# Optimization experiments

Measured on AMD Instinct MI355X. Metric: run time of the kernel, lower is better.

Reference implementation:

```python
import jax, jax.numpy as jnp
import numpy as np

NUM_HEADS = 8

B, N, M = 2, 10000, 320000
QD = KD = HD = 256


def setup_inputs() -> dict:
    key = jax.random.key(0)
    k1, k2, k3, k4, k5 = jax.random.split(key, 5)
    x_q = jax.random.normal(k1, (B, N, QD), dtype=jnp.float32)
    x_k = jax.random.normal(k2, (B, N, KD), dtype=jnp.float32)
    mask = jax.random.randint(k3, (2, M), 0, N, dtype=jnp.int64)
    # xavier_uniform: limit = sqrt(6/(fan_in+fan_out))
    lim_q = float(np.sqrt(6.0 / (QD + HD)))
    lim_k = float(np.sqrt(6.0 / (KD + HD)))
    w_q = jax.random.uniform(k4, (QD, HD), minval=-lim_q, maxval=lim_q, dtype=jnp.float32)
    w_k = jax.random.uniform(k5, (KD, HD), minval=-lim_k, maxval=lim_k, dtype=jnp.float32)
    return {"x_q": x_q, "x_k": x_k, "mask": mask, "w_q": w_q, "w_k": w_k}


def reference(x_q, x_k, mask, w_q, w_k):
    b, n, _ = x_q.shape
    m = mask.shape[1]
    d = w_q.shape[1]          # hidden_dim
    h = NUM_HEADS
    dh = d // h
    q = x_q @ w_q             # (b, n, d)
    k = x_k @ w_k             # (b, n, d)
    # edge gather + elementwise multiply
    prod = q[:, mask[0], :] * k[:, mask[1], :]            # (b, m, d)
    # head buffer is i // (d/h): contiguous blocks -> reshape-sum
    a = prod.reshape(b, m, h, dh).sum(axis=-1)            # (b, m, h)
    a = a / jnp.sqrt(jnp.float32(w_k.shape[0]))           # / sqrt(key_dim)
    # segment softmax over destination index = mask[1 - reduce_dim], reduce_dim=1 -> mask[0]
    idx = mask[0]
    a = a - a.max()                                       # global max, as in source
    e = jnp.exp(a)                                        # (b, m, h)
    seg = jnp.zeros((b, n, h), e.dtype).at[:, idx, :].add(e)
    return e / (seg[:, idx, :] + 1e-16)
```

## Files before the change

kernel.cpp:

```cpp
#include <hip/hip_runtime.h>
#include <hip/hip_bf16.h>
#include <hip/hip_fp16.h>

#define DHID 256
#define NHEAD 8
#define BATCH 2
#define PAD 96

typedef _Float16 h8 __attribute__((ext_vector_type(8)));
typedef _Float16 h2 __attribute__((ext_vector_type(2)));
typedef float f4 __attribute__((ext_vector_type(4)));
typedef int i2 __attribute__((ext_vector_type(2)));

__global__ __launch_bounds__(256) void prep_kernel(
    const float* __restrict__ Wq, const float* __restrict__ Wk,
    _Float16* __restrict__ Wfq, _Float16* __restrict__ Wfk,
    int* __restrict__ cnt, int N)
{
    if (blockIdx.z == 2) {
        const int gid = (blockIdx.y * 8 + blockIdx.x) * 256
                      + threadIdx.y * 32 + threadIdx.x;
        if (gid < N) cnt[gid] = 0;
        return;
    }
    const float* W = blockIdx.z ? Wk : Wq;
    _Float16* Wf   = blockIdx.z ? Wfk : Wfq;
    __shared__ float tile[32][33];
    const int tx = threadIdx.x;
    const int ty = threadIdx.y;
    const int n0 = blockIdx.x * 32;
    const int k0 = blockIdx.y * 32;
#pragma unroll
    for (int j = 0; j < 32; j += 8)
        tile[ty + j][tx] = W[(size_t)(k0 + ty + j) * DHID + n0 + tx];
    __syncthreads();
#pragma unroll
    for (int j = 0; j < 32; j += 8) {
        const int n = n0 + ty + j;
        const int k = k0 + tx;
        const size_t u = ((size_t)(n >> 4) * 32 + (k >> 3)) * 16 + (n & 15);
        Wf[u * 8 + (k & 7)] = (_Float16)tile[tx][ty + j];
    }
}

__global__ __launch_bounds__(256, 4) void gemm_mfma(
    const float* __restrict__ Xq, const float* __restrict__ Xk,
    const _Float16* __restrict__ Wfq, const _Float16* __restrict__ Wfk,
    _Float16* __restrict__ Qh, _Float16* __restrict__ Kh,
    const int* __restrict__ mask, int* __restrict__ cnt, int* __restrict__ sde,
    int nx, int Mrows, int M, int N)
{
    const int t = threadIdx.x;
    if ((int)blockIdx.x >= nx) {
        const int sb = ((int)blockIdx.x - nx) + (blockIdx.z ? 64 : 0);
        for (int e = sb * 256 + t; e < M; e += 128 * 256) {
            int s = mask[e];
            int r = atomicAdd(&cnt[s], 1);
            if (r < PAD) {
                i2 v; v[0] = mask[M + e]; v[1] = e;
                *(i2*)(sde + ((size_t)s * PAD + r) * 2) = v;
            }
        }
        return;
    }

    const float* X     = blockIdx.z ? Xk : Xq;
    const _Float16* Wf = blockIdx.z ? Wfk : Wfq;
    _Float16* C        = blockIdx.z ? Kh : Qh;

    const int lane = t & 63;
    const int wave = t >> 6;
    const int quad = lane >> 4;
    const int l16  = lane & 15;
    const int rowBase = blockIdx.x * 64;
    int arow = rowBase + wave * 16 + l16;
    if (arow >= Mrows) arow = Mrows - 1;

    h8 af[8];
#pragma unroll
    for (int kc = 0; kc < 8; ++kc) {
        const float* p = X + (size_t)arow * DHID + (kc * 4 + quad) * 8;
        f4 v0 = *(const f4*)p;
        f4 v1 = *(const f4*)(p + 4);
        h8 hv;
        hv[0]=(_Float16)v0[0]; hv[1]=(_Float16)v0[1]; hv[2]=(_Float16)v0[2]; hv[3]=(_Float16)v0[3];
        hv[4]=(_Float16)v1[0]; hv[5]=(_Float16)v1[1]; hv[6]=(_Float16)v1[2]; hv[7]=(_Float16)v1[3];
        af[kc] = hv;
    }

#pragma unroll 1
    for (int ct64 = 0; ct64 < 4; ++ct64) {
        f4 acc[4] = {{0,0,0,0},{0,0,0,0},{0,0,0,0},{0,0,0,0}};
#pragma unroll
        for (int kc = 0; kc < 8; ++kc) {
#pragma unroll
            for (int ct = 0; ct < 4; ++ct) {
                const h8 bf = *(const h8*)(Wf +
                    (((size_t)(ct64 * 4 + ct) * 32 + kc * 4 + quad) * 16 + l16) * 8);
                acc[ct] = __builtin_amdgcn_mfma_f32_16x16x32_f16(af[kc], bf, acc[ct], 0, 0, 0);
            }
        }
#pragma unroll
        for (int ct = 0; ct < 4; ++ct) {
#pragma unroll
            for (int r = 0; r < 4; ++r) {
                int grow = rowBase + wave * 16 + quad * 4 + r;
                if (grow < Mrows) {
                    int bb = grow >= N;
                    int nn = grow - (bb ? N : 0);
                    C[((size_t)nn * 2 + bb) * DHID + ct64 * 64 + ct * 16 + l16]
                        = (_Float16)acc[ct][r];
                }
            }
        }
    }
}

__global__ __launch_bounds__(256, 8) void edge_kernel(
    const _Float16* __restrict__ Qh, const _Float16* __restrict__ Kh,
    const int* __restrict__ cnt, const int* __restrict__ sde,
    float* __restrict__ out, int M, int N)
{
    __shared__ _Float16 evs[4][PAD][2][NHEAD];
    const int lane = threadIdx.x & 63;
    const int wave = threadIdx.x >> 6;
    const int c    = lane & 31;
    const int half = lane >> 5;
    const int h    = c >> 2;
    const int src  = blockIdx.x * 4 + wave;
    if (src >= N) return;
    int deg = cnt[src];
    if (deg > PAD) deg = PAD;
    if (deg == 0) return;
    const size_t base = (size_t)src * PAD;

    int dstv = 0, eidv = 0;
    if (lane < deg) {
        i2 v = *(const i2*)(sde + (base + lane) * 2);
        dstv = v[0]; eidv = v[1];
    }

    const _Float16* Qrow = Qh + (size_t)src * 2 * DHID;
    const h8 q0 = *(const h8*)(Qrow + c * 8);
    const h8 q1 = *(const h8*)(Qrow + DHID + c * 8);

    float seg0 = 0.f, seg1 = 0.f;
    for (int it = 0; it < deg; it += 8) {
        int pl[4], dd[4];
#pragma unroll
        for (int p = 0; p < 4; ++p) {
            pl[p] = it + p * 2 + half;
            if (it < 64) {
                dd[p] = __shfl(dstv, pl[p]);
            } else {
                int sc = pl[p] < deg ? pl[p] : deg - 1;
                dd[p] = sde[(base + sc) * 2];
            }
        }
        h8 k0v[4], k1v[4];
#pragma unroll
        for (int p = 0; p < 4; ++p) {
            const _Float16* Krow = Kh + (size_t)dd[p] * 2 * DHID;
            k0v[p] = *(const h8*)(Krow + c * 8);
            k1v[p] = *(const h8*)(Krow + DHID + c * 8);
        }
#pragma unroll
        for (int p = 0; p < 4; ++p) {
            float s0 = 0.f, s1 = 0.f;
#if __has_builtin(__builtin_amdgcn_fdot2)
#pragma unroll
            for (int u = 0; u < 4; ++u) {
                h2 a0, b0, a1, b1;
                a0[0] = q0[2*u];      a0[1] = q0[2*u+1];
                b0[0] = k0v[p][2*u];  b0[1] = k0v[p][2*u+1];
                a1[0] = q1[2*u];      a1[1] = q1[2*u+1];
                b1[0] = k1v[p][2*u];  b1[1] = k1v[p][2*u+1];
                s0 = __builtin_amdgcn_fdot2(a0, b0, s0, false);
                s1 = __builtin_amdgcn_fdot2(a1, b1, s1, false);
            }
#else
#pragma unroll
            for (int u = 0; u < 8; ++u) {
                s0 += (float)q0[u] * (float)k0v[p][u];
                s1 += (float)q1[u] * (float)k1v[p][u];
            }
#endif
            s0 += __shfl_xor(s0, 1); s0 += __shfl_xor(s0, 2);
            s1 += __shfl_xor(s1, 1); s1 += __shfl_xor(s1, 2);
            if ((c & 3) == 0 && pl[p] < deg) {
                _Float16 e0 = (_Float16)expf(s0 * 0.0625f);
                _Float16 e1 = (_Float16)expf(s1 * 0.0625f);
                evs[wave][pl[p]][0][h] = e0;
                evs[wave][pl[p]][1][h] = e1;
                seg0 += (float)e0; seg1 += (float)e1;
            }
        }
    }

    seg0 += __shfl_xor(seg0, 32);
    seg1 += __shfl_xor(seg1, 32);
    const float r0 = __builtin_amdgcn_rcpf(seg0 + 1e-16f);
    const float r1 = __builtin_amdgcn_rcpf(seg1 + 1e-16f);

    for (int it = 0; it < deg; it += 8) {
        int pl[4], ee[4];
#pragma unroll
        for (int p = 0; p < 4; ++p) {
            pl[p] = it + p * 2 + half;
            if (it < 64) {
                ee[p] = __shfl(eidv, pl[p]);
            } else {
                int sc = pl[p] < deg ? pl[p] : deg - 1;
                ee[p] = sde[(base + sc) * 2 + 1];
            }
        }
#pragma unroll
        for (int p = 0; p < 4; ++p) {
            if ((c & 3) == 0 && pl[p] < deg) {
                float v0 = (float)evs[wave][pl[p]][0][h] * r0;
                float v1 = (float)evs[wave][pl[p]][1][h] * r1;
                __builtin_nontemporal_store(v0, &out[(size_t)ee[p] * NHEAD + h]);
                __builtin_nontemporal_store(v1,
                    &out[(size_t)M * NHEAD + (size_t)ee[p] * NHEAD + h]);
            }
        }
    }
}

extern "C" void kernel_launch(void* const* d_in, const int* in_sizes, int n_in,
                              void* d_out, int out_size, void* d_ws, size_t ws_size,
                              hipStream_t stream) {
    const float* x_q  = (const float*)d_in[0];
    const float* x_k  = (const float*)d_in[1];
    const int*   mask = (const int*)d_in[2];
    const float* w_q  = (const float*)d_in[3];
    const float* w_k  = (const float*)d_in[4];
    float* out = (float*)d_out;

    const int M = in_sizes[2] / 2;
    const int N = in_sizes[0] / (BATCH * DHID);
    const int Mrows = BATCH * N;

    _Float16* Qh  = (_Float16*)d_ws;
    _Float16* Kh  = Qh  + (size_t)Mrows * DHID;
    _Float16* Wfq = Kh  + (size_t)Mrows * DHID;
    _Float16* Wfk = Wfq + (size_t)DHID * DHID;
    int*      cnt = (int*)(Wfk + (size_t)DHID * DHID);
    int*      sde = cnt + N;

    prep_kernel<<<dim3(DHID / 32, DHID / 32, 3), dim3(32, 8), 0, stream>>>(
        w_q, w_k, Wfq, Wfk, cnt, N);

    const int nx = (Mrows + 63) / 64;
    gemm_mfma<<<dim3(nx + 64, 1, 2), 256, 0, stream>>>(
        x_q, x_k, Wfq, Wfk, Qh, Kh, mask, cnt, sde, nx, Mrows, M, N);

    edge_kernel<<<dim3((N + 3) / 4), 256, 0, stream>>>(
        Qh, Kh, cnt, sde, out, M, N);
}
```

Measured before the change: 171.6 us.

## Prefetch next K-row gathers in edge kernel and split GEMM tiles across waves

The edge kernel now double-buffers its K-row gathers, loading the next group of 8 edges' K vectors before computing dot products on the current group. This hides gather latency at the cost of more registers, so the occupancy hint drops from 8 to 4 blocks. The exp call switches to the fast __expf intrinsic. The GEMM now gives each block 32 rows, with waves splitting the column tiles in pairs, which doubles the block count to spread the projection across more CUs.

After: 177.0 us. 1.03x slower.

```diff
diff --git a/kernel.cpp b/kernel.cpp
--- a/kernel.cpp
+++ b/kernel.cpp
@@ -72,8 +72,10 @@
     const int wave = t >> 6;
     const int quad = lane >> 4;
     const int l16  = lane & 15;
-    const int rowBase = blockIdx.x * 64;
-    int arow = rowBase + wave * 16 + l16;
+    const int rowHalf = wave & 1;
+    const int ctPair  = wave >> 1;
+    const int rowBase = blockIdx.x * 32;
+    int arow = rowBase + rowHalf * 16 + l16;
     if (arow >= Mrows) arow = Mrows - 1;
 
     h8 af[8];
@@ -88,8 +90,9 @@
         af[kc] = hv;
     }
 
-#pragma unroll 1
-    for (int ct64 = 0; ct64 < 4; ++ct64) {
+#pragma unroll
+    for (int cc = 0; cc < 2; ++cc) {
+        const int ct64 = ctPair * 2 + cc;
         f4 acc[4] = {{0,0,0,0},{0,0,0,0},{0,0,0,0},{0,0,0,0}};
 #pragma unroll
         for (int kc = 0; kc < 8; ++kc) {
@@ -104,7 +107,7 @@
         for (int ct = 0; ct < 4; ++ct) {
 #pragma unroll
             for (int r = 0; r < 4; ++r) {
-                int grow = rowBase + wave * 16 + quad * 4 + r;
+                int grow = rowBase + rowHalf * 16 + quad * 4 + r;
                 if (grow < Mrows) {
                     int bb = grow >= N;
                     int nn = grow - (bb ? N : 0);
@@ -116,7 +119,7 @@
     }
 }
 
-__global__ __launch_bounds__(256, 8) void edge_kernel(
+__global__ __launch_bounds__(256, 4) void edge_kernel(
     const _Float16* __restrict__ Qh, const _Float16* __restrict__ Kh,
     const int* __restrict__ cnt, const int* __restrict__ sde,
     float* __restrict__ out, int M, int N)
@@ -144,56 +147,74 @@
     const h8 q0 = *(const h8*)(Qrow + c * 8);
     const h8 q1 = *(const h8*)(Qrow + DHID + c * 8);
 
+    auto get_dd = [&](int it, int* dd) {
+#pragma unroll
+        for (int p = 0; p < 4; ++p) {
+            int pl = it + p * 2 + half;
+            if (it < 64) {
+                dd[p] = __shfl(dstv, pl);
+            } else {
+                int sc = pl < deg ? pl : deg - 1;
+                dd[p] = sde[(base + sc) * 2];
+            }
+        }
+    };
+    auto load_kv = [&](const int* dd, h8* ka, h8* kb) {
+#pragma unroll
+        for (int p = 0; p < 4; ++p) {
+            const _Float16* Krow = Kh + (size_t)dd[p] * 2 * DHID;
+            ka[p] = *(const h8*)(Krow + c * 8);
+            kb[p] = *(const h8*)(Krow + DHID + c * 8);
+        }
+    };
+
     float seg0 = 0.f, seg1 = 0.f;
+    int dd0[4]; h8 ka[4], kb[4];
+    get_dd(0, dd0);
+    load_kv(dd0, ka, kb);
+
     for (int it = 0; it < deg; it += 8) {
-        int pl[4], dd[4];
-#pragma unroll
-        for (int p = 0; p < 4; ++p) {
-            pl[p] = it + p * 2 + half;
-            if (it < 64) {
-                dd[p] = __shfl(dstv, pl[p]);
-            } else {
-                int sc = pl[p] < deg ? pl[p] : deg - 1;
-                dd[p] = sde[(base + sc) * 2];
-            }
-        }
-        h8 k0v[4], k1v[4];
-#pragma unroll
-        for (int p = 0; p < 4; ++p) {
-            const _Float16* Krow = Kh + (size_t)dd[p] * 2 * DHID;
-            k0v[p] = *(const h8*)(Krow + c * 8);
-            k1v[p] = *(const h8*)(Krow + DHID + c * 8);
-        }
-#pragma unroll
-        for (int p = 0; p < 4; ++p) {
+        const int itn = it + 8;
+        int dd1[4]; h8 kna[4], knb[4];
+        const bool more = itn < deg;
+        if (more) { get_dd(itn, dd1); load_kv(dd1, kna, knb); }
+
+#pragma unroll
+        for (int p = 0; p < 4; ++p) {
+            const int pl = it + p * 2 + half;
             float s0 = 0.f, s1 = 0.f;
 #if __has_builtin(__builtin_amdgcn_fdot2)
 #pragma unroll
             for (int u = 0; u < 4; ++u) {
                 h2 a0, b0, a1, b1;
-                a0[0] = q0[2*u];      a0[1] = q0[2*u+1];
-                b0[0] = k0v[p][2*u];  b0[1] = k0v[p][2*u+1];
-                a1[0] = q1[2*u];      a1[1] = q1[2*u+1];
-                b1[0] = k1v[p][2*u];  b1[1] = k1v[p][2*u+1];
+                a0[0] = q0[2*u];     a0[1] = q0[2*u+1];
+                b0[0] = ka[p][2*u];  b0[1] = ka[p][2*u+1];
+                a1[0] = q1[2*u];     a1[1] = q1[2*u+1];
+                b1[0] = kb[p][2*u];  b1[1] = kb[p][2*u+1];
                 s0 = __builtin_amdgcn_fdot2(a0, b0, s0, false);
                 s1 = __builtin_amdgcn_fdot2(a1, b1, s1, false);
             }
 #else
 #pragma unroll
             for (int u = 0; u < 8; ++u) {
-                s0 += (float)q0[u] * (float)k0v[p][u];
-                s1 += (float)q1[u] * (float)k1v[p][u];
+                s0 += (float)q0[u] * (float)ka[p][u];
+                s1 += (float)q1[u] * (float)kb[p][u];
             }
 #endif
             s0 += __shfl_xor(s0, 1); s0 += __shfl_xor(s0, 2);
             s1 += __shfl_xor(s1, 1); s1 += __shfl_xor(s1, 2);
-            if ((c & 3) == 0 && pl[p] < deg) {
-                _Float16 e0 = (_Float16)expf(s0 * 0.0625f);
-                _Float16 e1 = (_Float16)expf(s1 * 0.0625f);
-                evs[wave][pl[p]][0][h] = e0;
-                evs[wave][pl[p]][1][h] = e1;
+            if ((c & 3) == 0 && pl < deg) {
+                _Float16 e0 = (_Float16)__expf(s0 * 0.0625f);
+                _Float16 e1 = (_Float16)__expf(s1 * 0.0625f);
+                evs[wave][pl][0][h] = e0;
+                evs[wave][pl][1][h] = e1;
                 seg0 += (float)e0; seg1 += (float)e1;
             }
+        }
+
+        if (more) {
+#pragma unroll
+            for (int p = 0; p < 4; ++p) { ka[p] = kna[p]; kb[p] = knb[p]; }
         }
     }
 
@@ -251,7 +272,7 @@
     prep_kernel<<<dim3(DHID / 32, DHID / 32, 3), dim3(32, 8), 0, stream>>>(
         w_q, w_k, Wfq, Wfk, cnt, N);
 
-    const int nx = (Mrows + 63) / 64;
+    const int nx = (Mrows + 31) / 32;
     gemm_mfma<<<dim3(nx + 64, 1, 2), 256, 0, stream>>>(
         x_q, x_k, Wfq, Wfk, Qh, Kh, mask, cnt, sde, nx, Mrows, M, N);
 
```

## Split GEMM block into 32-row tiles with per-wave column pairs and double-buffered B loads

Applied to the files above, without the earlier changes.

Each GEMM block now covers 32 rows instead of 64, and its four waves split into two row halves times two column-pair groups, so every wave computes two 64-column tiles rather than four. B-fragment loads are double-buffered with explicit prefetch two k-steps ahead, to overlap global loads with MFMA work. The grid doubles and each X row is loaded by two waves, which raises redundant X traffic in exchange for more parallelism and less latency. The edge kernel also switches expf to the fast __expf intrinsic.

Result: slower. 176.6 us (+3.0%).

```diff
diff --git a/kernel.cpp b/kernel.cpp
--- a/kernel.cpp
+++ b/kernel.cpp
@@ -42,6 +42,22 @@
         Wf[u * 8 + (k & 7)] = (_Float16)tile[tx][ty + j];
     }
 }
+
+#define LOADB(c64, kc, dst)                                                     \
+    do {                                                                        \
+        dst[0] = *(const h8*)(Wf + ((((size_t)(c64) * 4 + 0) * 32 + (kc) * 4 + quad) * 16 + l16) * 8); \
+        dst[1] = *(const h8*)(Wf + ((((size_t)(c64) * 4 + 1) * 32 + (kc) * 4 + quad) * 16 + l16) * 8); \
+        dst[2] = *(const h8*)(Wf + ((((size_t)(c64) * 4 + 2) * 32 + (kc) * 4 + quad) * 16 + l16) * 8); \
+        dst[3] = *(const h8*)(Wf + ((((size_t)(c64) * 4 + 3) * 32 + (kc) * 4 + quad) * 16 + l16) * 8); \
+    } while (0)
+
+#define MFMA4(acc, kc, buf)                                                     \
+    do {                                                                        \
+        acc[0] = __builtin_amdgcn_mfma_f32_16x16x32_f16(af[kc], buf[0], acc[0], 0, 0, 0); \
+        acc[1] = __builtin_amdgcn_mfma_f32_16x16x32_f16(af[kc], buf[1], acc[1], 0, 0, 0); \
+        acc[2] = __builtin_amdgcn_mfma_f32_16x16x32_f16(af[kc], buf[2], acc[2], 0, 0, 0); \
+        acc[3] = __builtin_amdgcn_mfma_f32_16x16x32_f16(af[kc], buf[3], acc[3], 0, 0, 0); \
+    } while (0)
 
 __global__ __launch_bounds__(256, 4) void gemm_mfma(
     const float* __restrict__ Xq, const float* __restrict__ Xk,
@@ -72,8 +88,10 @@
     const int wave = t >> 6;
     const int quad = lane >> 4;
     const int l16  = lane & 15;
-    const int rowBase = blockIdx.x * 64;
-    int arow = rowBase + wave * 16 + l16;
+    const int rowHalf = wave & 1;
+    const int ctPair  = wave >> 1;
+    const int rowBase = blockIdx.x * 32;
+    int arow = rowBase + rowHalf * 16 + l16;
     if (arow >= Mrows) arow = Mrows - 1;
 
     h8 af[8];
@@ -88,29 +106,49 @@
         af[kc] = hv;
     }
 
-#pragma unroll 1
-    for (int ct64 = 0; ct64 < 4; ++ct64) {
-        f4 acc[4] = {{0,0,0,0},{0,0,0,0},{0,0,0,0},{0,0,0,0}};
-#pragma unroll
-        for (int kc = 0; kc < 8; ++kc) {
-#pragma unroll
-            for (int ct = 0; ct < 4; ++ct) {
-                const h8 bf = *(const h8*)(Wf +
-                    (((size_t)(ct64 * 4 + ct) * 32 + kc * 4 + quad) * 16 + l16) * 8);
-                acc[ct] = __builtin_amdgcn_mfma_f32_16x16x32_f16(af[kc], bf, acc[ct], 0, 0, 0);
-            }
-        }
-#pragma unroll
-        for (int ct = 0; ct < 4; ++ct) {
-#pragma unroll
-            for (int r = 0; r < 4; ++r) {
-                int grow = rowBase + wave * 16 + quad * 4 + r;
-                if (grow < Mrows) {
-                    int bb = grow >= N;
-                    int nn = grow - (bb ? N : 0);
-                    C[((size_t)nn * 2 + bb) * DHID + ct64 * 64 + ct * 16 + l16]
-                        = (_Float16)acc[ct][r];
-                }
+    const int c0 = ctPair * 2;
+    const int c1 = c0 + 1;
+    h8 bufA[4], bufB[4];
+    f4 acc0[4] = {{0,0,0,0},{0,0,0,0},{0,0,0,0},{0,0,0,0}};
+    f4 acc1[4] = {{0,0,0,0},{0,0,0,0},{0,0,0,0},{0,0,0,0}};
+
+    LOADB(c0, 0, bufA);
+    LOADB(c0, 1, bufB);
+
+#pragma unroll
+    for (int kc = 0; kc < 8; ++kc) {
+        if ((kc & 1) == 0) {
+            MFMA4(acc0, kc, bufA);
+            if (kc + 2 < 8) { LOADB(c0, kc + 2, bufA); }
+            else            { LOADB(c1, kc - 6, bufA); }
+        } else {
+            MFMA4(acc0, kc, bufB);
+            if (kc + 2 < 8) { LOADB(c0, kc + 2, bufB); }
+            else            { LOADB(c1, kc - 6, bufB); }
+        }
+    }
+#pragma unroll
+    for (int kc = 0; kc < 8; ++kc) {
+        if ((kc & 1) == 0) {
+            MFMA4(acc1, kc, bufA);
+            if (kc + 2 < 8) { LOADB(c1, kc + 2, bufA); }
+        } else {
+            MFMA4(acc1, kc, bufB);
+            if (kc + 2 < 8) { LOADB(c1, kc + 2, bufB); }
+        }
+    }
+
+#pragma unroll
+    for (int ct = 0; ct < 4; ++ct) {
+#pragma unroll
+        for (int r = 0; r < 4; ++r) {
+            int grow = rowBase + rowHalf * 16 + quad * 4 + r;
+            if (grow < Mrows) {
+                int bb = grow >= N;
+                int nn = grow - (bb ? N : 0);
+                size_t rowoff = ((size_t)nn * 2 + bb) * DHID;
+                C[rowoff + c0 * 64 + ct * 16 + l16] = (_Float16)acc0[ct][r];
+                C[rowoff + c1 * 64 + ct * 16 + l16] = (_Float16)acc1[ct][r];
             }
         }
     }
@@ -188,8 +226,8 @@
             s0 += __shfl_xor(s0, 1); s0 += __shfl_xor(s0, 2);
             s1 += __shfl_xor(s1, 1); s1 += __shfl_xor(s1, 2);
             if ((c & 3) == 0 && pl[p] < deg) {
-                _Float16 e0 = (_Float16)expf(s0 * 0.0625f);
-                _Float16 e1 = (_Float16)expf(s1 * 0.0625f);
+                _Float16 e0 = (_Float16)__expf(s0 * 0.0625f);
+                _Float16 e1 = (_Float16)__expf(s1 * 0.0625f);
                 evs[wave][pl[p]][0][h] = e0;
                 evs[wave][pl[p]][1][h] = e1;
                 seg0 += (float)e0; seg1 += (float)e1;
@@ -251,7 +289,7 @@
     prep_kernel<<<dim3(DHID / 32, DHID / 32, 3), dim3(32, 8), 0, stream>>>(
         w_q, w_k, Wfq, Wfk, cnt, N);
 
-    const int nx = (Mrows + 63) / 64;
+    const int nx = (Mrows + 31) / 32;
     gemm_mfma<<<dim3(nx + 64, 1, 2), 256, 0, stream>>>(
         x_q, x_k, Wfq, Wfk, Qh, Kh, mask, cnt, sde, nx, Mrows, M, N);
 
```

## Stage GEMM operands in swizzled LDS tiles instead of register/global fragments

Applied to the files above, without the earlier changes.

The projection GEMM now converts the 64x256 X tile to fp16 into XOR-swizzled shared memory. Per 64-column chunk it loads the plain transposed weight into shared memory as well, and MFMA fragments are read from LDS instead of directly from global memory in a pre-fragmented layout. The intent is cheaper, conflict-free operand fetches. In exchange it adds 64 KB of LDS per block, extra syncthreads, and lowers the launch-bounds occupancy hint to 2. The edge kernel also switches expf to the faster __expf intrinsic.

Result: no change. 169.9 us (-0.9%).

```diff
diff --git a/kernel.cpp b/kernel.cpp
--- a/kernel.cpp
+++ b/kernel.cpp
@@ -14,7 +14,7 @@
 
 __global__ __launch_bounds__(256) void prep_kernel(
     const float* __restrict__ Wq, const float* __restrict__ Wk,
-    _Float16* __restrict__ Wfq, _Float16* __restrict__ Wfk,
+    _Float16* __restrict__ Wtq, _Float16* __restrict__ Wtk,
     int* __restrict__ cnt, int N)
 {
     if (blockIdx.z == 2) {
@@ -24,7 +24,7 @@
         return;
     }
     const float* W = blockIdx.z ? Wk : Wq;
-    _Float16* Wf   = blockIdx.z ? Wfk : Wfq;
+    _Float16* Wt   = blockIdx.z ? Wtk : Wtq;
     __shared__ float tile[32][33];
     const int tx = threadIdx.x;
     const int ty = threadIdx.y;
@@ -35,17 +35,13 @@
         tile[ty + j][tx] = W[(size_t)(k0 + ty + j) * DHID + n0 + tx];
     __syncthreads();
 #pragma unroll
-    for (int j = 0; j < 32; j += 8) {
-        const int n = n0 + ty + j;
-        const int k = k0 + tx;
-        const size_t u = ((size_t)(n >> 4) * 32 + (k >> 3)) * 16 + (n & 15);
-        Wf[u * 8 + (k & 7)] = (_Float16)tile[tx][ty + j];
-    }
-}
-
-__global__ __launch_bounds__(256, 4) void gemm_mfma(
+    for (int j = 0; j < 32; j += 8)
+        Wt[(size_t)(n0 + ty + j) * DHID + k0 + tx] = (_Float16)tile[tx][ty + j];
+}
+
+__global__ __launch_bounds__(256, 2) void gemm_mfma(
     const float* __restrict__ Xq, const float* __restrict__ Xk,
-    const _Float16* __restrict__ Wfq, const _Float16* __restrict__ Wfk,
+    const _Float16* __restrict__ Wtq, const _Float16* __restrict__ Wtk,
     _Float16* __restrict__ Qh, _Float16* __restrict__ Kh,
     const int* __restrict__ mask, int* __restrict__ cnt, int* __restrict__ sde,
     int nx, int Mrows, int M, int N)
@@ -64,42 +60,65 @@
         return;
     }
 
-    const float* X     = blockIdx.z ? Xk : Xq;
-    const _Float16* Wf = blockIdx.z ? Wfk : Wfq;
-    _Float16* C        = blockIdx.z ? Kh : Qh;
+    const float* X       = blockIdx.z ? Xk : Xq;
+    const _Float16* Wt   = blockIdx.z ? Wtk : Wtq;
+    _Float16* C          = blockIdx.z ? Kh : Qh;
+
+    __shared__ _Float16 As[64 * 256];
+    __shared__ _Float16 Bs[64 * 256];
 
     const int lane = t & 63;
     const int wave = t >> 6;
-    const int quad = lane >> 4;
-    const int l16  = lane & 15;
     const int rowBase = blockIdx.x * 64;
-    int arow = rowBase + wave * 16 + l16;
-    if (arow >= Mrows) arow = Mrows - 1;
-
-    h8 af[8];
-#pragma unroll
-    for (int kc = 0; kc < 8; ++kc) {
-        const float* p = X + (size_t)arow * DHID + (kc * 4 + quad) * 8;
-        f4 v0 = *(const f4*)p;
-        f4 v1 = *(const f4*)(p + 4);
+
+#pragma unroll
+    for (int i = 0; i < 8; ++i) {
+        int idx = t + i * 256;
+        int row = idx >> 5;
+        int c   = idx & 31;
+        int grow = rowBase + row;
+        f4 v0 = {0,0,0,0}, v1 = {0,0,0,0};
+        if (grow < Mrows) {
+            const float* p = X + (size_t)grow * DHID + c * 8;
+            v0 = *(const f4*)p;
+            v1 = *(const f4*)(p + 4);
+        }
         h8 hv;
         hv[0]=(_Float16)v0[0]; hv[1]=(_Float16)v0[1]; hv[2]=(_Float16)v0[2]; hv[3]=(_Float16)v0[3];
         hv[4]=(_Float16)v1[0]; hv[5]=(_Float16)v1[1]; hv[6]=(_Float16)v1[2]; hv[7]=(_Float16)v1[3];
-        af[kc] = hv;
-    }
-
-#pragma unroll 1
+        int sc = c ^ (row & 7);
+        *(h8*)&As[row * 256 + sc * 8] = hv;
+    }
+
+    const int ar   = wave * 16 + (lane & 15);
+    const int quad = lane >> 4;
+
     for (int ct64 = 0; ct64 < 4; ++ct64) {
+#pragma unroll
+        for (int i = 0; i < 8; ++i) {
+            int idx = t + i * 256;
+            int n = idx >> 5;
+            int c = idx & 31;
+            h8 hv = *(const h8*)(Wt + (size_t)(ct64 * 64 + n) * DHID + c * 8);
+            int sc = c ^ (n & 7);
+            *(h8*)&Bs[n * 256 + sc * 8] = hv;
+        }
+        __syncthreads();
+
         f4 acc[4] = {{0,0,0,0},{0,0,0,0},{0,0,0,0},{0,0,0,0}};
 #pragma unroll
         for (int kc = 0; kc < 8; ++kc) {
+            int ac = (kc * 4 + quad) ^ (ar & 7);
+            h8 afrag = *(const h8*)&As[ar * 256 + ac * 8];
 #pragma unroll
             for (int ct = 0; ct < 4; ++ct) {
-                const h8 bf = *(const h8*)(Wf +
-                    (((size_t)(ct64 * 4 + ct) * 32 + kc * 4 + quad) * 16 + l16) * 8);
-                acc[ct] = __builtin_amdgcn_mfma_f32_16x16x32_f16(af[kc], bf, acc[ct], 0, 0, 0);
-            }
-        }
+                int bn = ct * 16 + (lane & 15);
+                int bc = (kc * 4 + quad) ^ (bn & 7);
+                h8 bfrag = *(const h8*)&Bs[bn * 256 + bc * 8];
+                acc[ct] = __builtin_amdgcn_mfma_f32_16x16x32_f16(afrag, bfrag, acc[ct], 0, 0, 0);
+            }
+        }
+
 #pragma unroll
         for (int ct = 0; ct < 4; ++ct) {
 #pragma unroll
@@ -108,11 +127,12 @@
                 if (grow < Mrows) {
                     int bb = grow >= N;
                     int nn = grow - (bb ? N : 0);
-                    C[((size_t)nn * 2 + bb) * DHID + ct64 * 64 + ct * 16 + l16]
+                    C[((size_t)nn * 2 + bb) * DHID + ct64 * 64 + ct * 16 + (lane & 15)]
                         = (_Float16)acc[ct][r];
                 }
             }
         }
+        __syncthreads();
     }
 }
 
@@ -188,8 +208,8 @@
             s0 += __shfl_xor(s0, 1); s0 += __shfl_xor(s0, 2);
             s1 += __shfl_xor(s1, 1); s1 += __shfl_xor(s1, 2);
             if ((c & 3) == 0 && pl[p] < deg) {
-                _Float16 e0 = (_Float16)expf(s0 * 0.0625f);
-                _Float16 e1 = (_Float16)expf(s1 * 0.0625f);
+                _Float16 e0 = (_Float16)__expf(s0 * 0.0625f);
+                _Float16 e1 = (_Float16)__expf(s1 * 0.0625f);
                 evs[wave][pl[p]][0][h] = e0;
                 evs[wave][pl[p]][1][h] = e1;
                 seg0 += (float)e0; seg1 += (float)e1;
@@ -243,17 +263,17 @@
 
     _Float16* Qh  = (_Float16*)d_ws;
     _Float16* Kh  = Qh  + (size_t)Mrows * DHID;
-    _Float16* Wfq = Kh  + (size_t)Mrows * DHID;
-    _Float16* Wfk = Wfq + (size_t)DHID * DHID;
-    int*      cnt = (int*)(Wfk + (size_t)DHID * DHID);
+    _Float16* Wtq = Kh  + (size_t)Mrows * DHID;
+    _Float16* Wtk = Wtq + (size_t)DHID * DHID;
+    int*      cnt = (int*)(Wtk + (size_t)DHID * DHID);
     int*      sde = cnt + N;
 
     prep_kernel<<<dim3(DHID / 32, DHID / 32, 3), dim3(32, 8), 0, stream>>>(
-        w_q, w_k, Wfq, Wfk, cnt, N);
+        w_q, w_k, Wtq, Wtk, cnt, N);
 
     const int nx = (Mrows + 63) / 64;
     gemm_mfma<<<dim3(nx + 64, 1, 2), 256, 0, stream>>>(
-        x_q, x_k, Wfq, Wfk, Qh, Kh, mask, cnt, sde, nx, Mrows, M, N);
+        x_q, x_k, Wtq, Wtk, Qh, Kh, mask, cnt, sde, nx, Mrows, M, N);
 
     edge_kernel<<<dim3((N + 3) / 4), 256, 0, stream>>>(
         Qh, Kh, cnt, sde, out, M, N);
```
